# Kernel optimization log

Hardware: AMD Instinct MI355X
Metric: run time of the kernel (lower is better)

Reference implementation:

```python
import jax, jax.numpy as jnp
import numpy as np

B, NQ, NK, DIM, H = 2, 2048, 4096, 256, 8
HD = DIM // H  # head dim = 32


def setup_inputs() -> dict:
    key = jax.random.key(0)
    ks = jax.random.split(key, 8)
    s = 0.02  # init scale for weights
    return {
        "xq": jax.random.normal(ks[0], (B, NQ, DIM), jnp.float32),
        "xk": jax.random.normal(ks[1], (B, NK, DIM), jnp.float32),
        "xv": jax.random.normal(ks[2], (B, NK, DIM), jnp.float32),
        # torch nn.Linear weights: shape (out, in), y = x @ W.T + b
        "wq": jax.random.normal(ks[3], (DIM, DIM), jnp.float32) * s,
        "wk": jax.random.normal(ks[4], (DIM, DIM), jnp.float32) * s,
        "wv": jax.random.normal(ks[5], (DIM, DIM), jnp.float32) * s,
        "wp": jax.random.normal(ks[6], (DIM, DIM), jnp.float32) * s,
        "bp": jnp.zeros((DIM,), jnp.float32),
    }


def reference(xq, xk, xv, wq, wk, wv, wp, bp):
    scale = HD ** (-0.5)
    Bq, Nq, C = xq.shape
    Nk = xk.shape[1]
    # project and split heads: [B, H, N, HD]
    q = jnp.einsum('bnc,dc->bnd', xq, wq).reshape(Bq, Nq, H, HD).transpose(0, 2, 1, 3)
    k = jnp.einsum('bnc,dc->bnd', xk, wk).reshape(Bq, Nk, H, HD).transpose(0, 2, 1, 3)
    v = jnp.einsum('bnc,dc->bnd', xv, wv).reshape(Bq, Nk, H, HD).transpose(0, 2, 1, 3)
    # pre-softmax scores [B, H, Nq, Nk]
    attn = jnp.einsum('bhqd,bhkd->bhqk', q, k) * scale
    attn_save = attn.sum(axis=1) / H  # head-mean of pre-softmax scores
    p = jax.nn.softmax(attn, axis=-1)
    x = jnp.einsum('bhqk,bhkd->bhqd', p, v).transpose(0, 2, 1, 3).reshape(Bq, Nq, C)
    x = jnp.einsum('bnc,dc->bnd', x, wp) + bp
    return x, attn_save
```

## Files before the change

### kernel.cpp

```cpp
#include <hip/hip_runtime.h>

typedef unsigned int u32;
typedef unsigned short u16;
typedef short bf16x8 __attribute__((ext_vector_type(8)));
typedef float f32x4 __attribute__((ext_vector_type(4)));
typedef float f32x8 __attribute__((ext_vector_type(8)));
typedef float f32x16 __attribute__((ext_vector_type(16)));
typedef int i32x4 __attribute__((ext_vector_type(4)));
typedef __bf16 bf16x2 __attribute__((ext_vector_type(2)));
typedef float f32x2 __attribute__((ext_vector_type(2)));
typedef _Float16 f16x2t __attribute__((ext_vector_type(2)));
typedef _Float16 f16x8 __attribute__((ext_vector_type(8)));

#define KSPLIT 4

__device__ __forceinline__ u32 pack2bf(float a, float b) {
    u32 ua = __float_as_uint(a), ub = __float_as_uint(b);
    ua = (ua + 0x7fffu + ((ua >> 16) & 1u)) >> 16;
    ub = (ub + 0x7fffu + ((ub >> 16) & 1u)) >> 16;
    return (ua & 0xffffu) | (ub << 16);
}
__device__ __forceinline__ u16 bf1(float a) {
    u32 ua = __float_as_uint(a);
    return (u16)((ua + 0x7fffu + ((ua >> 16) & 1u)) >> 16);
}
__device__ __forceinline__ u32 b2(float a, float b) {
    f32x2 f; f[0] = a; f[1] = b;
    bf16x2 h = __builtin_convertvector(f, bf16x2);
    return __builtin_bit_cast(u32, h);
}
__device__ __forceinline__ u32 h2(float a, float b) {
    f32x2 f; f[0] = a; f[1] = b;
    f16x2t h = __builtin_convertvector(f, f16x2t);
    return __builtin_bit_cast(u32, h);
}

__global__ __launch_bounds__(256) void cvt_w4(const float* __restrict__ wq,
                                              const float* __restrict__ wk,
                                              const float* __restrict__ wv,
                                              const float* __restrict__ wp,
                                              u16* __restrict__ dst) {
    int i = blockIdx.x * 256 + threadIdx.x;
    int which = i >> 14;
    int j = i & 16383;
    const float* s = which == 0 ? wq : which == 1 ? wk : which == 2 ? wv : wp;
    float4 a = ((const float4*)s)[j];
    uint2 v;
    v.x = pack2bf(a.x, a.y);
    v.y = pack2bf(a.z, a.w);
    ((uint2*)(dst + which * 65536))[j] = v;
}

__global__ __launch_bounds__(256) void proj_all(const float* __restrict__ xq,
                                                const float* __restrict__ xk,
                                                const float* __restrict__ xv,
                                                const u16* __restrict__ W4,
                                                u16* __restrict__ Qb,
                                                u16* __restrict__ K2,
                                                u16* __restrict__ V2,
                                                float qalpha) {
    int bx = blockIdx.x;
    int mode = bx < 64 ? 0 : (bx < 192 ? 1 : 2);
    int xb = mode == 0 ? bx : (mode == 1 ? bx - 64 : bx - 192);
    const float* X = mode == 0 ? xq : mode == 1 ? xk : xv;
    const u16* Wb = W4 + mode * 65536;

    __shared__ u16 xs[64 * 256];
    int t = threadIdx.x;
    int m0 = xb * 64;
#pragma unroll
    for (int i = 0; i < 8; i++) {
        int c16 = t + 256 * i;
        int row = c16 >> 5, col16 = c16 & 31;
        const float4* src = (const float4*)(X + (size_t)(m0 + row) * 256 + col16 * 8);
        float4 a = src[0], b2v = src[1];
        uint4 v;
        v.x = pack2bf(a.x, a.y); v.y = pack2bf(a.z, a.w);
        v.z = pack2bf(b2v.x, b2v.y); v.w = pack2bf(b2v.z, b2v.w);
        int byteoff = row * 512 + ((col16 * 16) ^ ((row & 7) << 4));
        *(uint4*)((char*)xs + byteoff) = v;
    }
    __syncthreads();
    int lane = t & 63, w = t >> 6;
    int lq = lane & 15, g = lane >> 4;
    int rowA = w * 16 + lq;
    f32x4 acc[16];
    f32x4 z = {0.f, 0.f, 0.f, 0.f};
#pragma unroll
    for (int nt = 0; nt < 16; nt++) acc[nt] = z;
#pragma unroll
    for (int kk = 0; kk < 8; kk++) {
        bf16x8 aF = *(const bf16x8*)((const char*)xs + rowA * 512 +
                                     ((kk * 64 + g * 16) ^ ((rowA & 7) << 4)));
#pragma unroll
        for (int nt = 0; nt < 16; nt++) {
            bf16x8 bF = *(const bf16x8*)(Wb + (size_t)(nt * 16 + lq) * 256 + kk * 32 + g * 8);
            acc[nt] = __builtin_amdgcn_mfma_f32_16x16x32_bf16(aF, bF, acc[nt], 0, 0, 0);
        }
    }
    if (mode == 0) {
#pragma unroll
        for (int nt = 0; nt < 16; nt++) {
            int col = nt * 16 + lq;
#pragma unroll
            for (int r = 0; r < 4; r++) {
                int m = m0 + w * 16 + g * 4 + r;
                Qb[(size_t)m * 256 + col] = bf1(acc[nt][r] * qalpha);
            }
        }
    } else if (mode == 1) {
        int m = m0 + w * 16 + g * 4;
        int b = m >> 12, n = m & 4095;
#pragma unroll
        for (int nt = 0; nt < 16; nt++) {
            int d = nt * 16 + lq;
            int h = d >> 5, d32 = d & 31;
            u16* p = K2 + ((size_t)(b * 8 + h) * 4096 + n) * 32 + d32;
#pragma unroll
            for (int r = 0; r < 4; r++) p[r * 32] = bf1(acc[nt][r]);
        }
    } else {
        int m = m0 + w * 16 + g * 4;
        int b = m >> 12, n = m & 4095;
        int s = n >> 5;
        int t5 = n & 31;
        int pklo = (t5 & 19) | ((t5 << 1) & 8) | ((t5 >> 1) & 4);
#pragma unroll
        for (int nt = 0; nt < 16; nt++) {
            int d = nt * 16 + lq;
            int h = d >> 5, d32 = d & 31;
            uint2 v;
            v.x = pack2bf(acc[nt][0], acc[nt][1]);
            v.y = pack2bf(acc[nt][2], acc[nt][3]);
            *(uint2*)(V2 + ((((size_t)(b * 8 + h) * 128 + s) * 32 + d32) * 32 + pklo)) = v;
        }
    }
}

__global__ __launch_bounds__(256) void save_gemm(const u16* __restrict__ Qb,
                                                 const u16* __restrict__ K2,
                                                 float* __restrict__ sv) {
    const float SAVE = 0.125f * 0.69314718055994530942f;
    int b = blockIdx.z;
    int m0 = blockIdx.y * 128, n0 = blockIdx.x * 128;
    int t = threadIdx.x, lane = t & 63, wv = t >> 6;
    int wr = wv >> 1, wc = wv & 1;
    int lq = lane & 15, g = lane >> 4;
    const u16* Q = Qb + (size_t)b * 2048 * 256;
    f32x4 acc[4][4];
    f32x4 z = {0.f, 0.f, 0.f, 0.f};
#pragma unroll
    for (int mt = 0; mt < 4; mt++)
#pragma unroll
        for (int nt = 0; nt < 4; nt++) acc[mt][nt] = z;
#pragma unroll
    for (int kk = 0; kk < 8; kk++) {
        bf16x8 aF[4], bF[4];
#pragma unroll
        for (int mt = 0; mt < 4; mt++)
            aF[mt] = *(const bf16x8*)(Q + (size_t)(m0 + wr * 64 + mt * 16 + lq) * 256 + kk * 32 + g * 8);
#pragma unroll
        for (int nt = 0; nt < 4; nt++)
            bF[nt] = *(const bf16x8*)(K2 + ((size_t)(b * 8 + kk) * 4096 + n0 + wc * 64 + nt * 16 + lq) * 32 + g * 8);
#pragma unroll
        for (int mt = 0; mt < 4; mt++)
#pragma unroll
            for (int nt = 0; nt < 4; nt++)
                acc[mt][nt] = __builtin_amdgcn_mfma_f32_16x16x32_bf16(aF[mt], bF[nt], acc[mt][nt], 0, 0, 0);
    }
#pragma unroll
    for (int mt = 0; mt < 4; mt++) {
#pragma unroll
        for (int nt = 0; nt < 4; nt++) {
            int col = n0 + wc * 64 + nt * 16 + lq;
#pragma unroll
            for (int r = 0; r < 4; r++) {
                int row = m0 + wr * 64 + mt * 16 + g * 4 + r;
                sv[((size_t)b * 2048 + row) * 4096 + col] = acc[mt][nt][r] * SAVE;
            }
        }
    }
}

__global__ __launch_bounds__(256, 2) void attn_part(const u16* __restrict__ Qb,
                                                    const u16* __restrict__ K2,
                                                    const u16* __restrict__ V2,
                                                    _Float16* __restrict__ PO,
                                                    float* __restrict__ PL) {
    int id = blockIdx.x;
    int h = id & 7;
    int r0 = id >> 3;
    int qblk = r0 & 7;
    int b = (r0 >> 3) & 1;
    int part = r0 >> 4;
    int bh = b * 8 + h;
    int t = threadIdx.x, lane = t & 63, w = t >> 6;
    int lq = lane & 31, hl = lane >> 5;
    int qa = qblk * 256 + w * 64 + lq;
    const u16* Qrow = Qb + ((size_t)(b * 2048 + qa)) * 256 + h * 32 + hl * 8;
    bf16x8 qf00 = *(const bf16x8*)(Qrow);
    bf16x8 qf01 = *(const bf16x8*)(Qrow + 16);
    bf16x8 qf10 = *(const bf16x8*)(Qrow + 32 * 256);
    bf16x8 qf11 = *(const bf16x8*)(Qrow + 32 * 256 + 16);
    const u16* Kh = K2 + ((size_t)bh * 4096 + part * 1024 + lq) * 32 + hl * 8;
    const u16* Vh = V2 + (size_t)bh * 131072 + part * 32768 + lq * 32 + hl * 8;
    f32x16 z16 = {};
    f32x16 o0 = z16, o1 = z16;
    float l0 = 0.f, l1 = 0.f;
    for (int it = 0; it < 16; ++it) {
#pragma unroll
        for (int s = 0; s < 2; s++) {
            const u16* kp = Kh + (it * 64 + s * 32) * 32;
            bf16x8 kf0 = *(const bf16x8*)(kp);
            bf16x8 kf1 = *(const bf16x8*)(kp + 16);
            const u16* vp = Vh + (it * 2 + s) * 1024;
            bf16x8 vf0 = *(const bf16x8*)(vp);
            bf16x8 vf1 = *(const bf16x8*)(vp + 16);
            f32x16 sA = __builtin_amdgcn_mfma_f32_32x32x16_bf16(kf0, qf00, z16, 0, 0, 0);
            sA = __builtin_amdgcn_mfma_f32_32x32x16_bf16(kf1, qf01, sA, 0, 0, 0);
            f32x16 sB = __builtin_amdgcn_mfma_f32_32x32x16_bf16(kf0, qf10, z16, 0, 0, 0);
            sB = __builtin_amdgcn_mfma_f32_32x32x16_bf16(kf1, qf11, sB, 0, 0, 0);
            float pA[16], pB[16];
#pragma unroll
            for (int k = 0; k < 16; k++) pA[k] = __builtin_amdgcn_exp2f(sA[k]);
#pragma unroll
            for (int k = 0; k < 16; k++) pB[k] = __builtin_amdgcn_exp2f(sB[k]);
            float la = 0.f, lb = 0.f;
#pragma unroll
            for (int k = 0; k < 16; k++) { la += pA[k]; lb += pB[k]; }
            l0 += la; l1 += lb;
            i32x4 wa0, wa1, wb0, wb1;
#pragma unroll
            for (int j = 0; j < 4; j++) {
                wa0[j] = (int)b2(pA[2 * j], pA[2 * j + 1]);
                wa1[j] = (int)b2(pA[8 + 2 * j], pA[9 + 2 * j]);
                wb0[j] = (int)b2(pB[2 * j], pB[2 * j + 1]);
                wb1[j] = (int)b2(pB[8 + 2 * j], pB[9 + 2 * j]);
            }
            bf16x8 pa0 = __builtin_bit_cast(bf16x8, wa0);
            bf16x8 pa1 = __builtin_bit_cast(bf16x8, wa1);
            bf16x8 pb0 = __builtin_bit_cast(bf16x8, wb0);
            bf16x8 pb1 = __builtin_bit_cast(bf16x8, wb1);
            o0 = __builtin_amdgcn_mfma_f32_32x32x16_bf16(vf0, pa0, o0, 0, 0, 0);
            o0 = __builtin_amdgcn_mfma_f32_32x32x16_bf16(vf1, pa1, o0, 0, 0, 0);
            o1 = __builtin_amdgcn_mfma_f32_32x32x16_bf16(vf0, pb0, o1, 0, 0, 0);
            o1 = __builtin_amdgcn_mfma_f32_32x32x16_bf16(vf1, pb1, o1, 0, 0, 0);
        }
    }
    l0 += __shfl_xor(l0, 32);
    l1 += __shfl_xor(l1, 32);
    size_t rowa = (size_t)(part * 16 + bh) * 2048 + qa;
    _Float16* poa = PO + rowa * 32;
    _Float16* pob = PO + (rowa + 32) * 32;
#pragma unroll
    for (int cc = 0; cc < 4; cc++) {
        uint2 va, vb;
        va.x = h2(o0[4 * cc + 0], o0[4 * cc + 1]);
        va.y = h2(o0[4 * cc + 2], o0[4 * cc + 3]);
        vb.x = h2(o1[4 * cc + 0], o1[4 * cc + 1]);
        vb.y = h2(o1[4 * cc + 2], o1[4 * cc + 3]);
        *(uint2*)(poa + cc * 8 + hl * 4) = va;
        *(uint2*)(pob + cc * 8 + hl * 4) = vb;
    }
    if (hl == 0) {
        PL[rowa] = l0;
        PL[rowa + 32] = l1;
    }
}

__global__ __launch_bounds__(256) void combine_oproj(const _Float16* __restrict__ PO,
                                                     const float* __restrict__ PL,
                                                     const u16* __restrict__ Wp,
                                                     const float* __restrict__ bp,
                                                     float* __restrict__ out) {
    __shared__ u16 os[16 * 256];
    int t = threadIdx.x;
    int qloc = t >> 4, chunk = t & 15;
    int R = blockIdx.x * 16 + qloc;
    int b = R >> 11, q = R & 2047;
    int h = chunk >> 1;
    int d0 = chunk * 16;
    int d32 = d0 & 31;
    int bh = b * 8 + h;
    float acc[16];
#pragma unroll
    for (int j = 0; j < 16; j++) acc[j] = 0.f;
    float L = 0.f;
#pragma unroll
    for (int p = 0; p < KSPLIT; p++) {
        size_t i = ((size_t)(p * 16 + bh) << 11) + q;
        L += PL[i];
        const f16x8* src = (const f16x8*)(PO + i * 32 + d32);
        f32x8 x0 = __builtin_convertvector(src[0], f32x8);
        f32x8 x1 = __builtin_convertvector(src[1], f32x8);
#pragma unroll
        for (int e = 0; e < 8; e++) { acc[e] += x0[e]; acc[8 + e] += x1[e]; }
    }
    float inv = 1.0f / L;
    uint4 w0, w1;
    w0.x = b2(acc[0] * inv, acc[1] * inv);   w0.y = b2(acc[2] * inv, acc[3] * inv);
    w0.z = b2(acc[4] * inv, acc[5] * inv);   w0.w = b2(acc[6] * inv, acc[7] * inv);
    w1.x = b2(acc[8] * inv, acc[9] * inv);   w1.y = b2(acc[10] * inv, acc[11] * inv);
    w1.z = b2(acc[12] * inv, acc[13] * inv); w1.w = b2(acc[14] * inv, acc[15] * inv);
    int col16a = d0 >> 3;
    *(uint4*)((char*)os + qloc * 512 + ((col16a * 16) ^ ((qloc & 7) << 4))) = w0;
    *(uint4*)((char*)os + qloc * 512 + (((col16a + 1) * 16) ^ ((qloc & 7) << 4))) = w1;
    __syncthreads();
    int lane = t & 63, w = t >> 6;
    int lq = lane & 15, g = lane >> 4;
    int nb = w * 4;
    f32x4 acc4[4];
    f32x4 z = {0.f, 0.f, 0.f, 0.f};
#pragma unroll
    for (int j = 0; j < 4; j++) acc4[j] = z;
#pragma unroll
    for (int kk = 0; kk < 8; kk++) {
        bf16x8 aF = *(const bf16x8*)((const char*)os + lq * 512 +
                                     ((kk * 64 + g * 16) ^ ((lq & 7) << 4)));
#pragma unroll
        for (int j = 0; j < 4; j++) {
            bf16x8 bF = *(const bf16x8*)(Wp + (size_t)((nb + j) * 16 + lq) * 256 + kk * 32 + g * 8);
            acc4[j] = __builtin_amdgcn_mfma_f32_16x16x32_bf16(aF, bF, acc4[j], 0, 0, 0);
        }
    }
    int R0 = blockIdx.x * 16;
#pragma unroll
    for (int j = 0; j < 4; j++) {
        int col = (nb + j) * 16 + lq;
        float bias = bp[col];
#pragma unroll
        for (int r = 0; r < 4; r++) {
            int row = R0 + g * 4 + r;
            out[(size_t)row * 256 + col] = acc4[j][r] + bias;
        }
    }
}

extern "C" void kernel_launch(void* const* d_in, const int* in_sizes, int n_in,
                              void* d_out, int out_size, void* d_ws, size_t ws_size,
                              hipStream_t stream) {
    const float* xq = (const float*)d_in[0];
    const float* xk = (const float*)d_in[1];
    const float* xv = (const float*)d_in[2];
    const float* wq = (const float*)d_in[3];
    const float* wk = (const float*)d_in[4];
    const float* wv = (const float*)d_in[5];
    const float* wp = (const float*)d_in[6];
    const float* bp = (const float*)d_in[7];
    float* out = (float*)d_out;

    u16* wsb = (u16*)d_ws;
    u16* W4 = wsb;
    u16* WPb = wsb + 196608;
    u16* Qb = wsb + 262144;
    u16* K2 = Qb + 1048576;
    u16* V2 = K2 + 2097152;

    float* outw = out + 1048576;
    _Float16* PO = (_Float16*)outw;
    float* PL = outw + 2097152;

    const float qalpha = 0.17677669529663687f * 1.4426950408889634f;

    cvt_w4<<<256, 256, 0, stream>>>(wq, wk, wv, wp, W4);
    proj_all<<<320, 256, 0, stream>>>(xq, xk, xv, W4, Qb, K2, V2, qalpha);

    attn_part<<<512, 256, 0, stream>>>(Qb, K2, V2, PO, PL);
    combine_oproj<<<256, 256, 0, stream>>>(PO, PL, WPb, bp, out);

    save_gemm<<<dim3(32, 16, 2), 256, 0, stream>>>(Qb, K2, out + 1048576);
}
```

Before: 114.1 us.

## Prefetch next K/V fragments and compute softmax row sums via MFMA with ones

Flattens the key loop into 32 steps and software-prefetches the next K and V fragments into registers while the current step computes. It also replaces the scalar VALU summation of exponentials and the final cross-lane shuffle with extra MFMAs that multiply a ones matrix by the bf16 probability fragments. The row-sum denominator now comes from the bf16-rounded probabilities, matching the values used in P@V. In exchange the matrix-core work per step grows from 8 to 12 MFMAs, and register pressure rises from the prefetch buffers and two more 16-wide accumulators.

Measured after the change: 111.1 us. 2.6% less time.

```diff
diff --git a/kernel.cpp b/kernel.cpp
--- a/kernel.cpp
+++ b/kernel.cpp
@@ -205,50 +205,52 @@
     const u16* Kh = K2 + ((size_t)bh * 4096 + part * 1024 + lq) * 32 + hl * 8;
     const u16* Vh = V2 + (size_t)bh * 131072 + part * 32768 + lq * 32 + hl * 8;
     f32x16 z16 = {};
-    f32x16 o0 = z16, o1 = z16;
-    float l0 = 0.f, l1 = 0.f;
-    for (int it = 0; it < 16; ++it) {
-#pragma unroll
-        for (int s = 0; s < 2; s++) {
-            const u16* kp = Kh + (it * 64 + s * 32) * 32;
-            bf16x8 kf0 = *(const bf16x8*)(kp);
-            bf16x8 kf1 = *(const bf16x8*)(kp + 16);
-            const u16* vp = Vh + (it * 2 + s) * 1024;
-            bf16x8 vf0 = *(const bf16x8*)(vp);
-            bf16x8 vf1 = *(const bf16x8*)(vp + 16);
-            f32x16 sA = __builtin_amdgcn_mfma_f32_32x32x16_bf16(kf0, qf00, z16, 0, 0, 0);
-            sA = __builtin_amdgcn_mfma_f32_32x32x16_bf16(kf1, qf01, sA, 0, 0, 0);
-            f32x16 sB = __builtin_amdgcn_mfma_f32_32x32x16_bf16(kf0, qf10, z16, 0, 0, 0);
-            sB = __builtin_amdgcn_mfma_f32_32x32x16_bf16(kf1, qf11, sB, 0, 0, 0);
-            float pA[16], pB[16];
-#pragma unroll
-            for (int k = 0; k < 16; k++) pA[k] = __builtin_amdgcn_exp2f(sA[k]);
-#pragma unroll
-            for (int k = 0; k < 16; k++) pB[k] = __builtin_amdgcn_exp2f(sB[k]);
-            float la = 0.f, lb = 0.f;
-#pragma unroll
-            for (int k = 0; k < 16; k++) { la += pA[k]; lb += pB[k]; }
-            l0 += la; l1 += lb;
-            i32x4 wa0, wa1, wb0, wb1;
-#pragma unroll
-            for (int j = 0; j < 4; j++) {
-                wa0[j] = (int)b2(pA[2 * j], pA[2 * j + 1]);
-                wa1[j] = (int)b2(pA[8 + 2 * j], pA[9 + 2 * j]);
-                wb0[j] = (int)b2(pB[2 * j], pB[2 * j + 1]);
-                wb1[j] = (int)b2(pB[8 + 2 * j], pB[9 + 2 * j]);
-            }
-            bf16x8 pa0 = __builtin_bit_cast(bf16x8, wa0);
-            bf16x8 pa1 = __builtin_bit_cast(bf16x8, wa1);
-            bf16x8 pb0 = __builtin_bit_cast(bf16x8, wb0);
-            bf16x8 pb1 = __builtin_bit_cast(bf16x8, wb1);
-            o0 = __builtin_amdgcn_mfma_f32_32x32x16_bf16(vf0, pa0, o0, 0, 0, 0);
-            o0 = __builtin_amdgcn_mfma_f32_32x32x16_bf16(vf1, pa1, o0, 0, 0, 0);
-            o1 = __builtin_amdgcn_mfma_f32_32x32x16_bf16(vf0, pb0, o1, 0, 0, 0);
-            o1 = __builtin_amdgcn_mfma_f32_32x32x16_bf16(vf1, pb1, o1, 0, 0, 0);
-        }
-    }
-    l0 += __shfl_xor(l0, 32);
-    l1 += __shfl_xor(l1, 32);
+    f32x16 o0 = z16, o1 = z16, laa = z16, lab = z16;
+    const short ONE = (short)0x3F80;
+    bf16x8 onesF = {ONE, ONE, ONE, ONE, ONE, ONE, ONE, ONE};
+    bf16x8 kf0 = *(const bf16x8*)(Kh);
+    bf16x8 kf1 = *(const bf16x8*)(Kh + 16);
+    bf16x8 vf0 = *(const bf16x8*)(Vh);
+    bf16x8 vf1 = *(const bf16x8*)(Vh + 16);
+    for (int i = 0; i < 32; ++i) {
+        int nx = i < 31 ? i + 1 : 31;
+        const u16* nkp = Kh + nx * 1024;
+        const u16* nvp = Vh + nx * 1024;
+        bf16x8 nk0 = *(const bf16x8*)(nkp);
+        bf16x8 nk1 = *(const bf16x8*)(nkp + 16);
+        bf16x8 nv0 = *(const bf16x8*)(nvp);
+        bf16x8 nv1 = *(const bf16x8*)(nvp + 16);
+        f32x16 sA = __builtin_amdgcn_mfma_f32_32x32x16_bf16(kf0, qf00, z16, 0, 0, 0);
+        sA = __builtin_amdgcn_mfma_f32_32x32x16_bf16(kf1, qf01, sA, 0, 0, 0);
+        f32x16 sB = __builtin_amdgcn_mfma_f32_32x32x16_bf16(kf0, qf10, z16, 0, 0, 0);
+        sB = __builtin_amdgcn_mfma_f32_32x32x16_bf16(kf1, qf11, sB, 0, 0, 0);
+        float pA[16], pB[16];
+#pragma unroll
+        for (int k = 0; k < 16; k++) pA[k] = __builtin_amdgcn_exp2f(sA[k]);
+#pragma unroll
+        for (int k = 0; k < 16; k++) pB[k] = __builtin_amdgcn_exp2f(sB[k]);
+        i32x4 wa0, wa1, wb0, wb1;
+#pragma unroll
+        for (int j = 0; j < 4; j++) {
+            wa0[j] = (int)b2(pA[2 * j], pA[2 * j + 1]);
+            wa1[j] = (int)b2(pA[8 + 2 * j], pA[9 + 2 * j]);
+            wb0[j] = (int)b2(pB[2 * j], pB[2 * j + 1]);
+            wb1[j] = (int)b2(pB[8 + 2 * j], pB[9 + 2 * j]);
+        }
+        bf16x8 pa0 = __builtin_bit_cast(bf16x8, wa0);
+        bf16x8 pa1 = __builtin_bit_cast(bf16x8, wa1);
+        bf16x8 pb0 = __builtin_bit_cast(bf16x8, wb0);
+        bf16x8 pb1 = __builtin_bit_cast(bf16x8, wb1);
+        laa = __builtin_amdgcn_mfma_f32_32x32x16_bf16(onesF, pa0, laa, 0, 0, 0);
+        laa = __builtin_amdgcn_mfma_f32_32x32x16_bf16(onesF, pa1, laa, 0, 0, 0);
+        lab = __builtin_amdgcn_mfma_f32_32x32x16_bf16(onesF, pb0, lab, 0, 0, 0);
+        lab = __builtin_amdgcn_mfma_f32_32x32x16_bf16(onesF, pb1, lab, 0, 0, 0);
+        o0 = __builtin_amdgcn_mfma_f32_32x32x16_bf16(vf0, pa0, o0, 0, 0, 0);
+        o0 = __builtin_amdgcn_mfma_f32_32x32x16_bf16(vf1, pa1, o0, 0, 0, 0);
+        o1 = __builtin_amdgcn_mfma_f32_32x32x16_bf16(vf0, pb0, o1, 0, 0, 0);
+        o1 = __builtin_amdgcn_mfma_f32_32x32x16_bf16(vf1, pb1, o1, 0, 0, 0);
+        kf0 = nk0; kf1 = nk1; vf0 = nv0; vf1 = nv1;
+    }
     size_t rowa = (size_t)(part * 16 + bh) * 2048 + qa;
     _Float16* poa = PO + rowa * 32;
     _Float16* pob = PO + (rowa + 32) * 32;
@@ -263,8 +265,8 @@
         *(uint2*)(pob + cc * 8 + hl * 4) = vb;
     }
     if (hl == 0) {
-        PL[rowa] = l0;
-        PL[rowa + 32] = l1;
+        PL[rowa] = laa[0];
+        PL[rowa + 32] = lab[0];
     }
 }
 
```
